# Kernel optimization log

Measured on AMD Instinct MI355X. Metric: run time of the kernel, lower is better.

## Reference

```python
import jax, jax.numpy as jnp
import numpy as np


def _gcn_conv(x, W, b, src, dst, n):
    # PyG GCNConv: add self-loops, symmetric normalization deg^{-1/2} A deg^{-1/2},
    # linear transform, scatter-add aggregation, bias.
    h = x @ W  # [N, H]
    # degree including self-loop (count of dst occurrences + 1)
    deg = jnp.zeros((n,), h.dtype).at[dst].add(1.0) + 1.0
    dinv = jax.lax.rsqrt(deg)  # deg^{-1/2}
    edge_norm = (dinv[src] * dinv[dst])[:, None]  # [E, 1]
    agg = jax.ops.segment_sum(h[src] * edge_norm, dst, num_segments=n)  # [N, H]
    # self-loop contribution: norm = dinv[i]*dinv[i]
    return agg + h * (dinv * dinv)[:, None] + b


def setup_inputs() -> dict:
    N, E, F_IN, HID, OUT = 100000, 1600000, 128, 128, 64
    key = jax.random.key(0)
    ks = jax.random.split(key, 8)
    x = jax.random.normal(ks[0], (N, F_IN), dtype=jnp.float32)
    edge_index = jax.random.randint(ks[1], (2, E), 0, N, dtype=jnp.int32)
    s1 = 1.0 / np.sqrt(F_IN)
    s2 = 1.0 / np.sqrt(HID)
    W1 = jax.random.uniform(ks[2], (F_IN, HID), jnp.float32, -s1, s1)
    b1 = jax.random.uniform(ks[3], (HID,), jnp.float32, -s1, s1)
    W2 = jax.random.uniform(ks[4], (HID, HID), jnp.float32, -s2, s2)
    b2 = jax.random.uniform(ks[5], (HID,), jnp.float32, -s2, s2)
    W_out = jax.random.uniform(ks[6], (HID, OUT), jnp.float32, -s2, s2)
    b_out = jax.random.uniform(ks[7], (OUT,), jnp.float32, -s2, s2)
    return {"x": x, "edge_index": edge_index, "W1": W1, "b1": b1,
            "W2": W2, "b2": b2, "W_out": W_out, "b_out": b_out}


def reference(x, edge_index, W1, b1, W2, b2, W_out, b_out):
    n = x.shape[0]
    src, dst = edge_index[0], edge_index[1]
    h = _gcn_conv(x, W1, b1, src, dst, n)
    h = jax.nn.relu(h)
    # F.dropout(training=self.training): identity in eval mode
    h = _gcn_conv(h, W2, b2, src, dst, n)
    h = jax.nn.relu(h)
    logits = h @ W_out + b_out
    return jax.nn.log_softmax(logits, axis=1)
```

## Files before the change

kernel.cpp:

```cpp
#include <hip/hip_runtime.h>
#include <hip/hip_bf16.h>


#define FEAT 128
#define OUTF 64
#define BSH 7
#define BNODES (1 << BSH)
#define SCHUNK_SH 12
#define SCHUNK (1 << SCHUNK_SH)
#define NREP 8
#define GDEPTH 16

typedef __attribute__((ext_vector_type(8))) short short8;
typedef __attribute__((ext_vector_type(4))) float f32x4;

__device__ __forceinline__ unsigned short bf16_rn(float f) {
    unsigned int u = __float_as_uint(f);
    u += 0x7FFFu + ((u >> 16) & 1u);
    return (unsigned short)(u >> 16);
}
__device__ __forceinline__ float bf16_lo(unsigned int u) { return __uint_as_float(u << 16); }
__device__ __forceinline__ float bf16_hi(unsigned int u) { return __uint_as_float(u & 0xFFFF0000u); }

__global__ __launch_bounds__(256) void bincount8_kernel(
        const int* __restrict__ dst, int* __restrict__ bcnt8, int E, int NB) {
    __shared__ int h[8192];
    int t = threadIdx.x;
    int nb8 = NB * NREP;
    for (int i = t; i < nb8; i += 256) h[i] = 0;
    __syncthreads();
    int stride = gridDim.x * 256;
    for (int e = blockIdx.x * 256 + t; e < E; e += stride) {
        int rep = (e >> SCHUNK_SH) & (NREP - 1);
        atomicAdd(&h[((dst[e] >> BSH) << 3) | rep], 1);
    }
    __syncthreads();
    for (int i = t; i < nb8; i += 256)
        if (h[i]) atomicAdd(&bcnt8[i], h[i]);
}

__global__ __launch_bounds__(1024) void bucket_scan8_kernel(
        const int* __restrict__ bcnt8, int* __restrict__ bcur8,
        int* __restrict__ bbase, int NB, int E) {
    int t = threadIdx.x;
    int nb8 = NB * NREP;
    int base = t * 8;
    int v[8];
    #pragma unroll
    for (int i = 0; i < 8; ++i) v[i] = (base + i < nb8) ? bcnt8[base + i] : 0;
    int local = 0;
    #pragma unroll
    for (int i = 0; i < 8; ++i) local += v[i];
    int lane = t & 63, wv = t >> 6;
    int x = local;
    #pragma unroll
    for (int o = 1; o < 64; o <<= 1) {
        int y = __shfl_up(x, o);
        if (lane >= o) x += y;
    }
    __shared__ int wsum[16];
    if (lane == 63) wsum[wv] = x;
    __syncthreads();
    int woff = 0;
    for (int i = 0; i < wv; ++i) woff += wsum[i];
    int run = woff + x - local;
    #pragma unroll
    for (int i = 0; i < 8; ++i) {
        int g = base + i;
        if (g < nb8) {
            bcur8[g] = run;
            if ((g & (NREP - 1)) == 0) bbase[g >> 3] = run;
        }
        run += v[i];
    }
    if (t == 0) bbase[NB] = E;
}

__global__ __launch_bounds__(256) void bin_scatter_kernel(
        const int* __restrict__ src, const int* __restrict__ dst,
        int* __restrict__ bcur8, unsigned int* __restrict__ staged,
        int E, int NB) {
    __shared__ int lcnt[1024];
    __shared__ int lbase[1024];
    int t = threadIdx.x;
    int rep = blockIdx.x & (NREP - 1);
    int e0 = blockIdx.x << SCHUNK_SH;
    int e1 = min(e0 + SCHUNK, E);
    for (int i = t; i < NB; i += 256) lcnt[i] = 0;
    __syncthreads();
    for (int e = e0 + t; e < e1; e += 256)
        atomicAdd(&lcnt[dst[e] >> BSH], 1);
    __syncthreads();
    for (int i = t; i < NB; i += 256) {
        int c = lcnt[i];
        lbase[i] = c ? atomicAdd(&bcur8[(i << 3) | rep], c) : 0;
        lcnt[i] = 0;
    }
    __syncthreads();
    for (int e = e0 + t; e < e1; e += 256) {
        int s = src[e], d = dst[e];
        int b = d >> BSH, dl = d & (BNODES - 1);
        int pos = lbase[b] + atomicAdd(&lcnt[b], 1);
        staged[pos] = (unsigned int)s | ((unsigned int)dl << 25);
    }
}

__global__ __launch_bounds__(256) void bucket_place_kernel(
        const unsigned int* __restrict__ staged, const int* __restrict__ bbase,
        int* __restrict__ row_ptr, float* __restrict__ dinv,
        int* __restrict__ csr_src, int N, int E) {
    int b = blockIdx.x;
    int t = threadIdx.x;
    int base = bbase[b], end = bbase[b + 1];
    __shared__ int cnt[BNODES];
    __shared__ int cur[BNODES];
    __shared__ int wsum2[2];
    if (t < BNODES) cnt[t] = 0;
    __syncthreads();
    for (int i = base + t; i < end; i += 256)
        atomicAdd(&cnt[staged[i] >> 25], 1);
    __syncthreads();

    bool act = t < BNODES;
    int v = act ? cnt[t] : 0;
    int lane = t & 63, wv = t >> 6;
    int x = v;
    #pragma unroll
    for (int o = 1; o < 64; o <<= 1) {
        int y = __shfl_up(x, o);
        if (lane >= o) x += y;
    }
    if (lane == 63 && wv == 0) wsum2[0] = x;
    __syncthreads();
    if (act) {
        int excl = x - v + (wv == 1 ? wsum2[0] : 0);
        int gnode = b * BNODES + t;
        int rp = base + excl;
        cur[t] = rp;
        if (gnode < N) {
            row_ptr[gnode] = rp;
            dinv[gnode] = rsqrtf((float)v + 1.0f);
        }
    }
    __syncthreads();
    for (int i = base + t; i < end; i += 256) {
        unsigned int u = staged[i];
        int dl = u >> 25;
        int p = atomicAdd(&cur[dl], 1);
        csr_src[p] = (int)(u & 0x1FFFFFFu);
    }
    if (b == 0 && t == 0) row_ptr[N] = E;
}

__global__ __launch_bounds__(256) void convw_kernel(
        const float* __restrict__ W1, const float* __restrict__ W2,
        const float* __restrict__ Wout,
        __hip_bfloat16* __restrict__ W1t, __hip_bfloat16* __restrict__ W2t,
        __hip_bfloat16* __restrict__ WoutT) {
    int idx = blockIdx.x * 256 + threadIdx.x;
    if (idx < 2 * FEAT * FEAT) {
        int which = idx >> 14;
        int r = idx & (FEAT * FEAT - 1);
        int n = r >> 7, k = r & 127;
        const float* W = which ? W2 : W1;
        unsigned short* Wt = (unsigned short*)(which ? W2t : W1t);
        Wt[r] = bf16_rn(W[k * FEAT + n]);
    } else if (idx < 2 * FEAT * FEAT + OUTF * FEAT) {
        int r = idx - 2 * FEAT * FEAT;
        int n = r >> 7, k = r & 127;
        ((unsigned short*)WoutT)[r] = bf16_rn(Wout[k * OUTF + n]);
    }
}

template <bool IN_FP32>
__global__ __launch_bounds__(256) void mfma_gemm_kernel(
        const void* __restrict__ Xv, const __hip_bfloat16* __restrict__ Wt,
        const float* __restrict__ dinv, __hip_bfloat16* __restrict__ Y, int N) {
    __shared__ short Ws[FEAT][136];
    int t = threadIdx.x;
    for (int i = t; i < FEAT * 16; i += 256) {
        int n = i >> 4, c = i & 15;
        *(uint4*)&Ws[n][c * 8] = *(const uint4*)((const unsigned short*)Wt + n * FEAT + c * 8);
    }
    __syncthreads();

    int wave = t >> 6, lane = t & 63;
    int m = lane & 15, quad = lane >> 4;
    int rbase = (blockIdx.x * 4 + wave) * 16;
    if (rbase >= N) return;
    int row = rbase + m;
    bool rok = row < N;

    f32x4 acc[8];
    #pragma unroll
    for (int nt = 0; nt < 8; ++nt) acc[nt] = (f32x4){0.f, 0.f, 0.f, 0.f};

    #pragma unroll
    for (int ks = 0; ks < 4; ++ks) {
        short8 a;
        if (IN_FP32) {
            const float* X = (const float*)Xv;
            float xs[8];
            if (rok) {
                float4 x0 = *(const float4*)(X + (size_t)row * FEAT + ks * 32 + quad * 8);
                float4 x1 = *(const float4*)(X + (size_t)row * FEAT + ks * 32 + quad * 8 + 4);
                xs[0] = x0.x; xs[1] = x0.y; xs[2] = x0.z; xs[3] = x0.w;
                xs[4] = x1.x; xs[5] = x1.y; xs[6] = x1.z; xs[7] = x1.w;
            } else {
                #pragma unroll
                for (int j = 0; j < 8; ++j) xs[j] = 0.f;
            }
            #pragma unroll
            for (int j = 0; j < 8; ++j) a[j] = (short)bf16_rn(xs[j]);
        } else {
            const unsigned short* X = (const unsigned short*)Xv;
            if (rok)
                a = *(const short8*)(X + (size_t)row * FEAT + ks * 32 + quad * 8);
            else {
                #pragma unroll
                for (int j = 0; j < 8; ++j) a[j] = 0;
            }
        }
        #pragma unroll
        for (int nt = 0; nt < 8; ++nt) {
            short8 bfr = *(const short8*)&Ws[nt * 16 + m][ks * 32 + quad * 8];
            acc[nt] = __builtin_amdgcn_mfma_f32_16x16x32_bf16(a, bfr, acc[nt], 0, 0, 0);
        }
    }

    float dr[4];
    #pragma unroll
    for (int r = 0; r < 4; ++r) {
        int ro = rbase + quad * 4 + r;
        dr[r] = (ro < N) ? dinv[ro] : 0.f;
    }
    unsigned short* Yo = (unsigned short*)Y;
    #pragma unroll
    for (int nt = 0; nt < 8; ++nt) {
        #pragma unroll
        for (int r = 0; r < 4; ++r) {
            int ro = rbase + quad * 4 + r;
            if (ro < N)
                Yo[(size_t)ro * FEAT + nt * 16 + m] = bf16_rn(acc[nt][r] * dr[r]);
        }
    }
}

template <int EPI>
__global__ __launch_bounds__(256, 4) void gather_fused_kernel(
        const int* __restrict__ row_ptr, const int* __restrict__ csr_src,
        const float* __restrict__ dinv, const __hip_bfloat16* __restrict__ Hs,
        const float* __restrict__ bias, const __hip_bfloat16* __restrict__ Wt,
        const float* __restrict__ bvec, void* __restrict__ outp, int N) {
    constexpr int WR = (EPI == 1) ? FEAT : OUTF;
    __shared__ short Ws[WR][136];
    __shared__ short As[16][136];

    int t = threadIdx.x;
    for (int i = t; i < WR * 16; i += 256) {
        int n = i >> 4, c = i & 15;
        *(uint4*)&Ws[n][c * 8] = *(const uint4*)((const unsigned short*)Wt + n * FEAT + c * 8);
    }

    int lane = t & 63;
    int wave = t >> 6;
    int grp = lane >> 4;
    int fl = lane & 15;
    int node = blockIdx.x * 16 + wave * 4 + grp;
    bool nok = node < N;
    int nd = nok ? node : 0;

    const char* Hb = (const char*)Hs;
    unsigned foff = (unsigned)fl << 4;

    uint4 hu = *(const uint4*)(Hb + (((unsigned)nd << 8) + foff));
    float di = dinv[nd];
    float4 b0 = ((const float4*)bias)[fl * 2];
    float4 b1 = ((const float4*)bias)[fl * 2 + 1];

    float acc[8];
    #pragma unroll
    for (int i = 0; i < 8; ++i) acc[i] = 0.f;

    int j = row_ptr[nd], end = row_ptr[nd + 1];

    for (; j + GDEPTH <= end; j += GDEPTH) {
        unsigned off[GDEPTH];
        #pragma unroll
        for (int k = 0; k < GDEPTH; ++k)
            off[k] = ((unsigned)csr_src[j + k] << 8) + foff;
        uint4 u[GDEPTH];
        #pragma unroll
        for (int k = 0; k < GDEPTH; ++k)
            u[k] = *(const uint4*)(Hb + off[k]);
        #pragma unroll
        for (int k = 0; k < GDEPTH; ++k) {
            acc[0] += bf16_lo(u[k].x); acc[1] += bf16_hi(u[k].x);
            acc[2] += bf16_lo(u[k].y); acc[3] += bf16_hi(u[k].y);
            acc[4] += bf16_lo(u[k].z); acc[5] += bf16_hi(u[k].z);
            acc[6] += bf16_lo(u[k].w); acc[7] += bf16_hi(u[k].w);
        }
    }
    if (j < end) {
        int mm = end - j;
        unsigned off[GDEPTH];
        #pragma unroll
        for (int k = 0; k < GDEPTH; ++k)
            off[k] = ((unsigned)csr_src[j + (k < mm ? k : 0)] << 8) + foff;
        uint4 u[GDEPTH];
        #pragma unroll
        for (int k = 0; k < GDEPTH; ++k)
            u[k] = *(const uint4*)(Hb + off[k]);
        #pragma unroll
        for (int k = 0; k < GDEPTH; ++k) {
            if (k < mm) {
                acc[0] += bf16_lo(u[k].x); acc[1] += bf16_hi(u[k].x);
                acc[2] += bf16_lo(u[k].y); acc[3] += bf16_hi(u[k].y);
                acc[4] += bf16_lo(u[k].z); acc[5] += bf16_hi(u[k].z);
                acc[6] += bf16_lo(u[k].w); acc[7] += bf16_hi(u[k].w);
            }
        }
    }

    acc[0] += bf16_lo(hu.x); acc[1] += bf16_hi(hu.x);
    acc[2] += bf16_lo(hu.y); acc[3] += bf16_hi(hu.y);
    acc[4] += bf16_lo(hu.z); acc[5] += bf16_hi(hu.z);
    acc[6] += bf16_lo(hu.w); acc[7] += bf16_hi(hu.w);

    float v0 = fmaxf(di * acc[0] + b0.x, 0.f);
    float v1 = fmaxf(di * acc[1] + b0.y, 0.f);
    float v2 = fmaxf(di * acc[2] + b0.z, 0.f);
    float v3 = fmaxf(di * acc[3] + b0.w, 0.f);
    float v4 = fmaxf(di * acc[4] + b1.x, 0.f);
    float v5 = fmaxf(di * acc[5] + b1.y, 0.f);
    float v6 = fmaxf(di * acc[6] + b1.z, 0.f);
    float v7 = fmaxf(di * acc[7] + b1.w, 0.f);

    uint4 o;
    o.x = (unsigned int)bf16_rn(v0) | ((unsigned int)bf16_rn(v1) << 16);
    o.y = (unsigned int)bf16_rn(v2) | ((unsigned int)bf16_rn(v3) << 16);
    o.z = (unsigned int)bf16_rn(v4) | ((unsigned int)bf16_rn(v5) << 16);
    o.w = (unsigned int)bf16_rn(v6) | ((unsigned int)bf16_rn(v7) << 16);

    *(uint4*)&As[wave * 4 + grp][fl * 8] = o;
    __syncthreads();

    int m = lane & 15, quad = lane >> 4;
    int rbase0 = blockIdx.x * 16;

    if (EPI == 1) {
        f32x4 acc2[2];
        #pragma unroll
        for (int n2 = 0; n2 < 2; ++n2) acc2[n2] = (f32x4){0.f, 0.f, 0.f, 0.f};
        #pragma unroll
        for (int ks = 0; ks < 4; ++ks) {
            short8 a = *(const short8*)&As[m][ks * 32 + quad * 8];
            #pragma unroll
            for (int n2 = 0; n2 < 2; ++n2) {
                int nt = wave * 2 + n2;
                short8 bfr = *(const short8*)&Ws[nt * 16 + m][ks * 32 + quad * 8];
                acc2[n2] = __builtin_amdgcn_mfma_f32_16x16x32_bf16(a, bfr, acc2[n2], 0, 0, 0);
            }
        }
        unsigned short* Yo = (unsigned short*)outp;
        #pragma unroll
        for (int r = 0; r < 4; ++r) {
            int ro = rbase0 + quad * 4 + r;
            if (ro < N) {
                float dr = dinv[ro];
                #pragma unroll
                for (int n2 = 0; n2 < 2; ++n2)
                    Yo[(size_t)ro * FEAT + (wave * 2 + n2) * 16 + m] =
                        bf16_rn(acc2[n2][r] * dr);
            }
        }
    } else {
        if (wave == 0) {
            f32x4 acc4[4];
            #pragma unroll
            for (int nt = 0; nt < 4; ++nt) acc4[nt] = (f32x4){0.f, 0.f, 0.f, 0.f};
            #pragma unroll
            for (int ks = 0; ks < 4; ++ks) {
                short8 a = *(const short8*)&As[m][ks * 32 + quad * 8];
                #pragma unroll
                for (int nt = 0; nt < 4; ++nt) {
                    short8 bfr = *(const short8*)&Ws[nt * 16 + m][ks * 32 + quad * 8];
                    acc4[nt] = __builtin_amdgcn_mfma_f32_16x16x32_bf16(a, bfr, acc4[nt], 0, 0, 0);
                }
            }
            float bj[4];
            #pragma unroll
            for (int nt = 0; nt < 4; ++nt) bj[nt] = bvec[nt * 16 + m];
            float* out = (float*)outp;
            #pragma unroll
            for (int r = 0; r < 4; ++r) {
                int ro = rbase0 + quad * 4 + r;
                if (ro >= N) continue;
                float w0 = acc4[0][r] + bj[0];
                float w1 = acc4[1][r] + bj[1];
                float w2 = acc4[2][r] + bj[2];
                float w3 = acc4[3][r] + bj[3];
                float mx = fmaxf(fmaxf(w0, w1), fmaxf(w2, w3));
                #pragma unroll
                for (int os = 1; os <= 8; os <<= 1) mx = fmaxf(mx, __shfl_xor(mx, os));
                float s = __expf(w0 - mx) + __expf(w1 - mx) + __expf(w2 - mx) + __expf(w3 - mx);
                #pragma unroll
                for (int os = 1; os <= 8; os <<= 1) s += __shfl_xor(s, os);
                float ls = mx + __logf(s);
                float* op = out + (size_t)ro * OUTF + m;
                op[0]  = w0 - ls;
                op[16] = w1 - ls;
                op[32] = w2 - ls;
                op[48] = w3 - ls;
            }
        }
    }
}

extern "C" void kernel_launch(void* const* d_in, const int* in_sizes, int n_in,
                              void* d_out, int out_size, void* d_ws, size_t ws_size,
                              hipStream_t stream) {
    const float* x    = (const float*)d_in[0];
    const int*   ei   = (const int*)  d_in[1];
    const float* W1   = (const float*)d_in[2];
    const float* b1   = (const float*)d_in[3];
    const float* W2   = (const float*)d_in[4];
    const float* b2   = (const float*)d_in[5];
    const float* Wout = (const float*)d_in[6];
    const float* bout = (const float*)d_in[7];
    float* out = (float*)d_out;

    int N = in_sizes[0] / FEAT;
    int E = in_sizes[1] / 2;
    const int* srcp = ei;
    const int* dstp = ei + E;
    int NB = (N + BNODES - 1) >> BSH;

    char* ws = (char*)d_ws;
    __hip_bfloat16* Bh   = (__hip_bfloat16*)ws;
    __hip_bfloat16* Ba   = Bh + (size_t)N * FEAT;
    __hip_bfloat16* W1t  = Ba + (size_t)N * FEAT;
    __hip_bfloat16* W2t  = W1t + FEAT * FEAT;
    __hip_bfloat16* WoutT = W2t + FEAT * FEAT;
    float* dinv    = (float*)(WoutT + OUTF * FEAT);
    int*   rowp    = (int*)(dinv + N);
    int*   bcnt8   = rowp + N + 1;
    int*   bcur8   = bcnt8 + 8192;
    int*   bbase   = bcur8 + 8192;
    unsigned int* staged = (unsigned int*)(bbase + 1032);
    int*   csrsrc  = (int*)(staged + E);

    hipMemsetAsync(bcnt8, 0, (size_t)NB * NREP * sizeof(int), stream);
    bincount8_kernel<<<256, 256, 0, stream>>>(dstp, bcnt8, E, NB);
    bucket_scan8_kernel<<<1, 1024, 0, stream>>>(bcnt8, bcur8, bbase, NB, E);
    bin_scatter_kernel<<<(E + SCHUNK - 1) / SCHUNK, 256, 0, stream>>>(
        srcp, dstp, bcur8, staged, E, NB);
    bucket_place_kernel<<<NB, 256, 0, stream>>>(staged, bbase, rowp, dinv, csrsrc, N, E);
    convw_kernel<<<(2 * FEAT * FEAT + OUTF * FEAT + 255) / 256, 256, 0, stream>>>(
        W1, W2, Wout, W1t, W2t, WoutT);

    int ggrid = (N + 63) / 64;
    int agrid = (N + 15) / 16;

    mfma_gemm_kernel<true><<<ggrid, 256, 0, stream>>>(x, W1t, dinv, Bh, N);

    gather_fused_kernel<1><<<agrid, 256, 0, stream>>>(
        rowp, csrsrc, dinv, Bh, b1, W2t, nullptr, Ba, N);

    gather_fused_kernel<2><<<agrid, 256, 0, stream>>>(
        rowp, csrsrc, dinv, Ba, b2, WoutT, bout, out, N);
}
```

Before: 323.6 us.

## Replace bucketed CSR build with global-atomic degree count, three-pass scan, direct placement

Replaces the two-level bucketed counting sort (LDS bin counts, staged buffer, per-bucket placement) with a direct CSR build. Per-node degrees are counted with global atomics, fused with the weight conversion. A three-kernel scan then builds row_ptr, cursors and dinv, and each edge is placed straight into csr_src with a global atomic. This drops the staged intermediate buffer and one pass over the edges, at the cost of heavily contended global atomics and a scattered, non-deterministic order of neighbors inside each row.

```diff
diff --git a/kernel.cpp b/kernel.cpp
--- a/kernel.cpp
+++ b/kernel.cpp
@@ -4,11 +4,6 @@
 
 #define FEAT 128
 #define OUTF 64
-#define BSH 7
-#define BNODES (1 << BSH)
-#define SCHUNK_SH 12
-#define SCHUNK (1 << SCHUNK_SH)
-#define NREP 8
 #define GDEPTH 16
 
 typedef __attribute__((ext_vector_type(8))) short short8;
@@ -22,153 +17,121 @@
 __device__ __forceinline__ float bf16_lo(unsigned int u) { return __uint_as_float(u << 16); }
 __device__ __forceinline__ float bf16_hi(unsigned int u) { return __uint_as_float(u & 0xFFFF0000u); }
 
-__global__ __launch_bounds__(256) void bincount8_kernel(
-        const int* __restrict__ dst, int* __restrict__ bcnt8, int E, int NB) {
-    __shared__ int h[8192];
-    int t = threadIdx.x;
-    int nb8 = NB * NREP;
-    for (int i = t; i < nb8; i += 256) h[i] = 0;
-    __syncthreads();
-    int stride = gridDim.x * 256;
-    for (int e = blockIdx.x * 256 + t; e < E; e += stride) {
-        int rep = (e >> SCHUNK_SH) & (NREP - 1);
-        atomicAdd(&h[((dst[e] >> BSH) << 3) | rep], 1);
-    }
-    __syncthreads();
-    for (int i = t; i < nb8; i += 256)
-        if (h[i]) atomicAdd(&bcnt8[i], h[i]);
-}
-
-__global__ __launch_bounds__(1024) void bucket_scan8_kernel(
-        const int* __restrict__ bcnt8, int* __restrict__ bcur8,
-        int* __restrict__ bbase, int NB, int E) {
-    int t = threadIdx.x;
-    int nb8 = NB * NREP;
-    int base = t * 8;
-    int v[8];
-    #pragma unroll
-    for (int i = 0; i < 8; ++i) v[i] = (base + i < nb8) ? bcnt8[base + i] : 0;
-    int local = 0;
-    #pragma unroll
-    for (int i = 0; i < 8; ++i) local += v[i];
-    int lane = t & 63, wv = t >> 6;
-    int x = local;
-    #pragma unroll
-    for (int o = 1; o < 64; o <<= 1) {
-        int y = __shfl_up(x, o);
-        if (lane >= o) x += y;
-    }
-    __shared__ int wsum[16];
-    if (lane == 63) wsum[wv] = x;
-    __syncthreads();
-    int woff = 0;
-    for (int i = 0; i < wv; ++i) woff += wsum[i];
-    int run = woff + x - local;
-    #pragma unroll
-    for (int i = 0; i < 8; ++i) {
-        int g = base + i;
-        if (g < nb8) {
-            bcur8[g] = run;
-            if ((g & (NREP - 1)) == 0) bbase[g >> 3] = run;
-        }
-        run += v[i];
-    }
-    if (t == 0) bbase[NB] = E;
-}
-
-__global__ __launch_bounds__(256) void bin_scatter_kernel(
-        const int* __restrict__ src, const int* __restrict__ dst,
-        int* __restrict__ bcur8, unsigned int* __restrict__ staged,
-        int E, int NB) {
-    __shared__ int lcnt[1024];
-    __shared__ int lbase[1024];
-    int t = threadIdx.x;
-    int rep = blockIdx.x & (NREP - 1);
-    int e0 = blockIdx.x << SCHUNK_SH;
-    int e1 = min(e0 + SCHUNK, E);
-    for (int i = t; i < NB; i += 256) lcnt[i] = 0;
-    __syncthreads();
-    for (int e = e0 + t; e < e1; e += 256)
-        atomicAdd(&lcnt[dst[e] >> BSH], 1);
-    __syncthreads();
-    for (int i = t; i < NB; i += 256) {
-        int c = lcnt[i];
-        lbase[i] = c ? atomicAdd(&bcur8[(i << 3) | rep], c) : 0;
-        lcnt[i] = 0;
-    }
-    __syncthreads();
-    for (int e = e0 + t; e < e1; e += 256) {
-        int s = src[e], d = dst[e];
-        int b = d >> BSH, dl = d & (BNODES - 1);
-        int pos = lbase[b] + atomicAdd(&lcnt[b], 1);
-        staged[pos] = (unsigned int)s | ((unsigned int)dl << 25);
-    }
-}
-
-__global__ __launch_bounds__(256) void bucket_place_kernel(
-        const unsigned int* __restrict__ staged, const int* __restrict__ bbase,
-        int* __restrict__ row_ptr, float* __restrict__ dinv,
-        int* __restrict__ csr_src, int N, int E) {
-    int b = blockIdx.x;
-    int t = threadIdx.x;
-    int base = bbase[b], end = bbase[b + 1];
-    __shared__ int cnt[BNODES];
-    __shared__ int cur[BNODES];
-    __shared__ int wsum2[2];
-    if (t < BNODES) cnt[t] = 0;
-    __syncthreads();
-    for (int i = base + t; i < end; i += 256)
-        atomicAdd(&cnt[staged[i] >> 25], 1);
-    __syncthreads();
-
-    bool act = t < BNODES;
-    int v = act ? cnt[t] : 0;
-    int lane = t & 63, wv = t >> 6;
-    int x = v;
-    #pragma unroll
-    for (int o = 1; o < 64; o <<= 1) {
-        int y = __shfl_up(x, o);
-        if (lane >= o) x += y;
-    }
-    if (lane == 63 && wv == 0) wsum2[0] = x;
-    __syncthreads();
-    if (act) {
-        int excl = x - v + (wv == 1 ? wsum2[0] : 0);
-        int gnode = b * BNODES + t;
-        int rp = base + excl;
-        cur[t] = rp;
-        if (gnode < N) {
-            row_ptr[gnode] = rp;
-            dinv[gnode] = rsqrtf((float)v + 1.0f);
-        }
-    }
-    __syncthreads();
-    for (int i = base + t; i < end; i += 256) {
-        unsigned int u = staged[i];
-        int dl = u >> 25;
-        int p = atomicAdd(&cur[dl], 1);
-        csr_src[p] = (int)(u & 0x1FFFFFFu);
-    }
-    if (b == 0 && t == 0) row_ptr[N] = E;
-}
-
-__global__ __launch_bounds__(256) void convw_kernel(
+__global__ __launch_bounds__(256) void degcount_conv_kernel(
+        const int* __restrict__ dst, int* __restrict__ deg, int E,
         const float* __restrict__ W1, const float* __restrict__ W2,
         const float* __restrict__ Wout,
         __hip_bfloat16* __restrict__ W1t, __hip_bfloat16* __restrict__ W2t,
         __hip_bfloat16* __restrict__ WoutT) {
-    int idx = blockIdx.x * 256 + threadIdx.x;
-    if (idx < 2 * FEAT * FEAT) {
-        int which = idx >> 14;
-        int r = idx & (FEAT * FEAT - 1);
-        int n = r >> 7, k = r & 127;
-        const float* W = which ? W2 : W1;
-        unsigned short* Wt = (unsigned short*)(which ? W2t : W1t);
-        Wt[r] = bf16_rn(W[k * FEAT + n]);
-    } else if (idx < 2 * FEAT * FEAT + OUTF * FEAT) {
-        int r = idx - 2 * FEAT * FEAT;
-        int n = r >> 7, k = r & 127;
-        ((unsigned short*)WoutT)[r] = bf16_rn(Wout[k * OUTF + n]);
+    int t = threadIdx.x;
+    if (blockIdx.x < 160) {
+        int idx = blockIdx.x * 256 + t;
+        if (idx < 2 * FEAT * FEAT) {
+            int which = idx >> 14;
+            int r = idx & (FEAT * FEAT - 1);
+            int n = r >> 7, k = r & 127;
+            const float* W = which ? W2 : W1;
+            unsigned short* Wt = (unsigned short*)(which ? W2t : W1t);
+            Wt[r] = bf16_rn(W[k * FEAT + n]);
+        } else if (idx < 2 * FEAT * FEAT + OUTF * FEAT) {
+            int r = idx - 2 * FEAT * FEAT;
+            int n = r >> 7, k = r & 127;
+            ((unsigned short*)WoutT)[r] = bf16_rn(Wout[k * OUTF + n]);
+        }
+    }
+    int stride = gridDim.x * 256;
+    for (int e = blockIdx.x * 256 + t; e < E; e += stride)
+        atomicAdd(&deg[dst[e]], 1);
+}
+
+__global__ __launch_bounds__(256) void scanA_kernel(
+        const int* __restrict__ deg, int* __restrict__ bsum, int N) {
+    int b = blockIdx.x, t = threadIdx.x;
+    int C = (N + 255) >> 8;
+    int base = b * C;
+    int cnt = min(C, N - base);
+    int s = 0;
+    for (int i = t; i < cnt; i += 256) s += deg[base + i];
+    #pragma unroll
+    for (int o = 1; o < 64; o <<= 1) s += __shfl_xor(s, o);
+    __shared__ int ws[4];
+    int lane = t & 63, wv = t >> 6;
+    if (lane == 0) ws[wv] = s;
+    __syncthreads();
+    if (t == 0) bsum[b] = ws[0] + ws[1] + ws[2] + ws[3];
+}
+
+__global__ __launch_bounds__(256) void scanB_kernel(
+        const int* __restrict__ bsum, int* __restrict__ boff,
+        int* __restrict__ row_ptr, int N, int E) {
+    int t = threadIdx.x;
+    int v = bsum[t];
+    int x = v;
+    int lane = t & 63, wv = t >> 6;
+    #pragma unroll
+    for (int o = 1; o < 64; o <<= 1) {
+        int y = __shfl_up(x, o);
+        if (lane >= o) x += y;
+    }
+    __shared__ int ws[4];
+    if (lane == 63) ws[wv] = x;
+    __syncthreads();
+    int woff = 0;
+    for (int i = 0; i < wv; ++i) woff += ws[i];
+    boff[t] = woff + x - v;
+    if (t == 0) row_ptr[N] = E;
+}
+
+__global__ __launch_bounds__(256) void scanC_kernel(
+        const int* __restrict__ deg, const int* __restrict__ boff,
+        int* __restrict__ row_ptr, int* __restrict__ cur,
+        float* __restrict__ dinv, int N) {
+    int b = blockIdx.x, t = threadIdx.x;
+    int C = (N + 255) >> 8;
+    int base = b * C;
+    int cnt = min(C, N - base);
+    int tc = (C + 255) >> 8;
+    int v[4];
+    int tsum = 0;
+    #pragma unroll 4
+    for (int j = 0; j < tc; ++j) {
+        int i = t * tc + j;
+        v[j] = (i < cnt) ? deg[base + i] : 0;
+        tsum += v[j];
+    }
+    int lane = t & 63, wv = t >> 6;
+    int x = tsum;
+    #pragma unroll
+    for (int o = 1; o < 64; o <<= 1) {
+        int y = __shfl_up(x, o);
+        if (lane >= o) x += y;
+    }
+    __shared__ int ws[4];
+    if (lane == 63) ws[wv] = x;
+    __syncthreads();
+    int woff = 0;
+    for (int i = 0; i < wv; ++i) woff += ws[i];
+    int run = boff[b] + woff + x - tsum;
+    #pragma unroll 4
+    for (int j = 0; j < tc; ++j) {
+        int i = t * tc + j;
+        if (i < cnt) {
+            int g = base + i;
+            row_ptr[g] = run;
+            cur[g] = run;
+            dinv[g] = rsqrtf((float)v[j] + 1.0f);
+            run += v[j];
+        }
+    }
+}
+
+__global__ __launch_bounds__(256) void place_kernel(
+        const int* __restrict__ src, const int* __restrict__ dst,
+        int* __restrict__ cur, int* __restrict__ csr_src, int E) {
+    int stride = gridDim.x * 256;
+    for (int e = blockIdx.x * 256 + threadIdx.x; e < E; e += stride) {
+        int p = atomicAdd(&cur[dst[e]], 1);
+        csr_src[p] = src[e];
     }
 }
 
@@ -434,7 +397,6 @@
     int E = in_sizes[1] / 2;
     const int* srcp = ei;
     const int* dstp = ei + E;
-    int NB = (N + BNODES - 1) >> BSH;
 
     char* ws = (char*)d_ws;
     __hip_bfloat16* Bh   = (__hip_bfloat16*)ws;
@@ -444,20 +406,19 @@
     __hip_bfloat16* WoutT = W2t + FEAT * FEAT;
     float* dinv    = (float*)(WoutT + OUTF * FEAT);
     int*   rowp    = (int*)(dinv + N);
-    int*   bcnt8   = rowp + N + 1;
-    int*   bcur8   = bcnt8 + 8192;
-    int*   bbase   = bcur8 + 8192;
-    unsigned int* staged = (unsigned int*)(bbase + 1032);
-    int*   csrsrc  = (int*)(staged + E);
-
-    hipMemsetAsync(bcnt8, 0, (size_t)NB * NREP * sizeof(int), stream);
-    bincount8_kernel<<<256, 256, 0, stream>>>(dstp, bcnt8, E, NB);
-    bucket_scan8_kernel<<<1, 1024, 0, stream>>>(bcnt8, bcur8, bbase, NB, E);
-    bin_scatter_kernel<<<(E + SCHUNK - 1) / SCHUNK, 256, 0, stream>>>(
-        srcp, dstp, bcur8, staged, E, NB);
-    bucket_place_kernel<<<NB, 256, 0, stream>>>(staged, bbase, rowp, dinv, csrsrc, N, E);
-    convw_kernel<<<(2 * FEAT * FEAT + OUTF * FEAT + 255) / 256, 256, 0, stream>>>(
-        W1, W2, Wout, W1t, W2t, WoutT);
+    int*   deg     = rowp + N + 1;
+    int*   cur     = deg + N;
+    int*   bsum    = cur + N;
+    int*   boff    = bsum + 256;
+    int*   csrsrc  = boff + 256;
+
+    hipMemsetAsync(deg, 0, (size_t)N * sizeof(int), stream);
+    degcount_conv_kernel<<<1024, 256, 0, stream>>>(
+        dstp, deg, E, W1, W2, Wout, W1t, W2t, WoutT);
+    scanA_kernel<<<256, 256, 0, stream>>>(deg, bsum, N);
+    scanB_kernel<<<1, 256, 0, stream>>>(bsum, boff, rowp, N, E);
+    scanC_kernel<<<256, 256, 0, stream>>>(deg, boff, rowp, cur, dinv, N);
+    place_kernel<<<1024, 256, 0, stream>>>(srcp, dstp, cur, csrsrc, E);
 
     int ggrid = (N + 63) / 64;
     int agrid = (N + 15) / 16;
```

Result: slower. 454.5 us (+40.5%).
